# Kernel optimization log

Hardware: AMD Instinct MI355X
Metric: run time of the kernel (lower is better)

The kernel has to match this reference:

```python
import jax, jax.numpy as jnp
import numpy as np

T, B, E, H = 2048, 2, 1024, 16
HD = E // H
EPS = 1e-5


def setup_inputs() -> dict:
    key = jax.random.key(0)
    k1, k2, k3 = jax.random.split(key, 3)
    bound_in = float(np.sqrt(6.0 / (3 * E + E)))   # xavier_uniform for [3E,E]
    bound_out = float(np.sqrt(6.0 / (E + E)))      # xavier_uniform for [E,E]
    return {
        "query": jax.random.normal(k1, (T, B, E), dtype=jnp.float32),
        "gamma": jnp.ones((E,), dtype=jnp.float32),
        "beta": jnp.zeros((E,), dtype=jnp.float32),
        "in_proj_weight": jax.random.uniform(k2, (3 * E, E), jnp.float32, -bound_in, bound_in),
        "out_proj_weight": jax.random.uniform(k3, (E, E), jnp.float32, -bound_out, bound_out),
    }


def reference(query, gamma, beta, in_proj_weight, out_proj_weight):
    # LayerNorm over channel dim
    mean = jnp.mean(query, axis=-1, keepdims=True)
    var = jnp.mean(jnp.square(query - mean), axis=-1, keepdims=True)
    ln = (query - mean) * jax.lax.rsqrt(var + EPS) * gamma + beta  # [T,B,E]

    # Fused QKV projection (no bias): qkv = ln @ W^T, W: [3E, E]
    qkv = jnp.einsum("tbe,fe->tbf", ln, in_proj_weight)  # [T,B,3E]
    q, k, v = jnp.split(qkv, 3, axis=-1)
    q = q.reshape(T, B, H, HD) * (HD ** -0.5)
    k = k.reshape(T, B, H, HD)
    v = v.reshape(T, B, H, HD)

    # Attention: scores [B,H,T,T]
    scores = jnp.einsum("tbhd,sbhd->bhts", q, k)
    attn = jax.nn.softmax(scores, axis=-1)
    ctx = jnp.einsum("bhts,sbhd->tbhd", attn, v).reshape(T, B, E)

    # Output projection + residual add (dropout prob = 0)
    out = jnp.einsum("tbe,fe->tbf", ctx, out_proj_weight)
    return query + out
```

## Files before the change

### kernel.cpp

```cpp
#include <hip/hip_runtime.h>
#include <hip/hip_bf16.h>
#include <math.h>

#define T_DIM 2048
#define B_DIM 2
#define E_DIM 1024
#define H_DIM 16
#define HD_DIM 64
#define M_DIM (T_DIM * B_DIM)
#define BH_DIM (B_DIM * H_DIM)

using bf16x8 = __attribute__((ext_vector_type(8))) __bf16;
using u16x8  = __attribute__((ext_vector_type(8))) unsigned short;
using f32x4  = __attribute__((ext_vector_type(4))) float;

static __device__ __forceinline__ unsigned short f2bf(float f) {
  unsigned u = __builtin_bit_cast(unsigned, f);
  u += 0x7fff + ((u >> 16) & 1);
  return (unsigned short)(u >> 16);
}

__device__ __forceinline__ void gload_lds16(const void* g, void* l) {
  __builtin_amdgcn_global_load_lds(
      (const __attribute__((address_space(1))) unsigned int*)g,
      (__attribute__((address_space(3))) unsigned int*)l, 16, 0, 0);
}

__global__ __launch_bounds__(256) void prep_kernel(
    const float* __restrict__ q, const float* __restrict__ gamma,
    const float* __restrict__ beta, unsigned short* __restrict__ ln_out,
    const float* __restrict__ w1, unsigned short* __restrict__ o1, int n1,
    const float* __restrict__ w2, unsigned short* __restrict__ o2, int n2) {
  int blk = blockIdx.x;
  int tid = threadIdx.x;
  if (blk >= M_DIM) {
    int i = (blk - M_DIM) * 256 + tid;
    const float* in; unsigned short* out; int idx;
    if (i < n1) { in = w1; out = o1; idx = i; }
    else if (i < n1 + n2) { in = w2; out = o2; idx = i - n1; }
    else return;
    float4 v = ((const float4*)in)[idx];
    ushort4 o;
    o.x = f2bf(v.x); o.y = f2bf(v.y); o.z = f2bf(v.z); o.w = f2bf(v.w);
    ((ushort4*)out)[idx] = o;
    return;
  }
  int row = blk;
  const float4* qr = (const float4*)(q + (size_t)row * E_DIM);
  float4 x = qr[tid];
  float s  = x.x + x.y + x.z + x.w;
  float ss = x.x * x.x + x.y * x.y + x.z * x.z + x.w * x.w;
#pragma unroll
  for (int off = 32; off >= 1; off >>= 1) {
    s  += __shfl_xor(s, off, 64);
    ss += __shfl_xor(ss, off, 64);
  }
  __shared__ float red[8];
  int wid = tid >> 6, lane = tid & 63;
  if (lane == 0) { red[wid] = s; red[4 + wid] = ss; }
  __syncthreads();
  s  = red[0] + red[1] + red[2] + red[3];
  ss = red[4] + red[5] + red[6] + red[7];
  float mean = s * (1.0f / E_DIM);
  float var  = ss * (1.0f / E_DIM) - mean * mean;
  float rstd = rsqrtf(var + 1e-5f);
  float4 g4 = ((const float4*)gamma)[tid];
  float4 b4 = ((const float4*)beta)[tid];
  ushort4 o;
  o.x = f2bf((x.x - mean) * rstd * g4.x + b4.x);
  o.y = f2bf((x.y - mean) * rstd * g4.y + b4.y);
  o.z = f2bf((x.z - mean) * rstd * g4.z + b4.z);
  o.w = f2bf((x.w - mean) * rstd * g4.w + b4.w);
  ((ushort4*)(ln_out + (size_t)row * E_DIM))[tid] = o;
}

__global__ __launch_bounds__(512) void gemm0_kernel(
    const unsigned short* __restrict__ A, const unsigned short* __restrict__ Bw,
    unsigned short* __restrict__ out_qkv) {
  __shared__ alignas(16) unsigned short lds[65536];
  int tid = threadIdx.x;
  int wid = tid >> 6, lane = tid & 63;
  int wm = wid >> 2, wn = wid & 3;
  int g = lane >> 4, lr = lane & 15;
  int m0 = blockIdx.y * 256, n0 = blockIdx.x * 256;
  f32x4 acc[8][4] = {};
  bf16x8 bfr[4][2];

  int srl  = tid >> 3;
  int scol = ((tid & 7) ^ (srl & 7)) * 8;
  int koff0 = ((0 * 4 + g) ^ (lr & 7)) * 8;
  int koff1 = ((1 * 4 + g) ^ (lr & 7)) * 8;
  int bhalf = wn >> 1;
  int brow  = (wn & 1) * 64;

#define STAGE_HALF(PTR, GR0, KT, LBASE)                                        \
  do {                                                                         \
    gload_lds16((PTR) + (size_t)((GR0) + srl) * E_DIM + (size_t)(KT) * 64 + scol, \
                lds + (LBASE) + (size_t)tid * 8);                              \
    gload_lds16((PTR) + (size_t)((GR0) + 64 + srl) * E_DIM + (size_t)(KT) * 64 + scol, \
                lds + (LBASE) + 4096 + (size_t)tid * 8);                       \
  } while (0)

#define AOFF(D, MR, KK) (((D) * 2 + wm) * 8192 + ((MR) * 16 + lr) * 64 + ((KK) ? koff1 : koff0))
#define BOFF(D, NF, KK) (32768 + ((D) * 2 + bhalf) * 8192 + (brow + (NF) * 16 + lr) * 64 + ((KK) ? koff1 : koff0))

#define PHASE(Q, D, DOB, VW, ...)                                              \
  do {                                                                         \
    bf16x8 af[2][2];                                                           \
    _Pragma("unroll")                                                          \
    for (int mi = 0; mi < 2; ++mi) {                                           \
      af[mi][0] = *(const bf16x8*)(lds + AOFF(D, 2 * (Q) + mi, 0));            \
      af[mi][1] = *(const bf16x8*)(lds + AOFF(D, 2 * (Q) + mi, 1));            \
    }                                                                          \
    if (DOB) {                                                                 \
      _Pragma("unroll")                                                        \
      for (int nf = 0; nf < 4; ++nf) {                                         \
        bfr[nf][0] = *(const bf16x8*)(lds + BOFF(D, nf, 0));                   \
        bfr[nf][1] = *(const bf16x8*)(lds + BOFF(D, nf, 1));                   \
      }                                                                        \
    }                                                                          \
    __VA_ARGS__;                                                               \
    VW;                                                                        \
    __builtin_amdgcn_s_barrier();                                              \
    __builtin_amdgcn_sched_barrier(0);                                         \
    __builtin_amdgcn_s_setprio(1);                                             \
    _Pragma("unroll")                                                          \
    for (int mi = 0; mi < 2; ++mi)                                             \
      _Pragma("unroll")                                                        \
      for (int nf = 0; nf < 4; ++nf) {                                         \
        acc[2 * (Q) + mi][nf] = __builtin_amdgcn_mfma_f32_16x16x32_bf16(       \
            af[mi][0], bfr[nf][0], acc[2 * (Q) + mi][nf], 0, 0, 0);            \
        acc[2 * (Q) + mi][nf] = __builtin_amdgcn_mfma_f32_16x16x32_bf16(       \
            af[mi][1], bfr[nf][1], acc[2 * (Q) + mi][nf], 0, 0, 0);            \
      }                                                                        \
    __builtin_amdgcn_s_setprio(0);                                             \
    __builtin_amdgcn_s_barrier();                                              \
    __builtin_amdgcn_sched_barrier(0);                                         \
  } while (0)

#define VMC4 asm volatile("s_waitcnt vmcnt(4)" ::: "memory")
#define VMC0 asm volatile("s_waitcnt vmcnt(0)" ::: "memory")
#define NOWAIT ((void)0)

  STAGE_HALF(Bw, n0,       0, 32768);
  STAGE_HALF(Bw, n0 + 128, 0, 40960);
  STAGE_HALF(A,  m0,       0, 0);
  STAGE_HALF(A,  m0 + 128, 0, 8192);
  STAGE_HALF(Bw, n0,       1, 49152);
  STAGE_HALF(Bw, n0 + 128, 1, 57344);
  VMC0;
  __builtin_amdgcn_s_barrier();
  __builtin_amdgcn_sched_barrier(0);

  for (int i = 0; i < 7; ++i) {
    int k1 = 2 * i + 1, k2 = 2 * i + 2, k3 = 2 * i + 3;
    PHASE(0, 0, true,  NOWAIT, STAGE_HALF(A,  m0,       k1, 16384));
    PHASE(1, 0, false, NOWAIT, STAGE_HALF(A,  m0 + 128, k1, 24576));
    PHASE(2, 0, false, NOWAIT, STAGE_HALF(Bw, n0,       k2, 32768));
    PHASE(3, 0, false, VMC4,   STAGE_HALF(Bw, n0 + 128, k2, 40960));
    PHASE(0, 1, true,  NOWAIT, STAGE_HALF(A,  m0,       k2, 0));
    PHASE(1, 1, false, NOWAIT, STAGE_HALF(A,  m0 + 128, k2, 8192));
    PHASE(2, 1, false, NOWAIT, STAGE_HALF(Bw, n0,       k3, 49152));
    PHASE(3, 1, false, VMC4,   STAGE_HALF(Bw, n0 + 128, k3, 57344));
  }
  PHASE(0, 0, true,  NOWAIT, STAGE_HALF(A,  m0,       15, 16384));
  PHASE(1, 0, false, NOWAIT, STAGE_HALF(A,  m0 + 128, 15, 24576));
  PHASE(2, 0, false, NOWAIT, );
  PHASE(3, 0, false, VMC0,   );
  PHASE(0, 1, true,  NOWAIT, );
  PHASE(1, 1, false, NOWAIT, );
  PHASE(2, 1, false, NOWAIT, );
  PHASE(3, 1, false, NOWAIT, );
#undef PHASE
#undef STAGE_HALF
#undef AOFF
#undef BOFF
#undef VMC4
#undef VMC0
#undef NOWAIT

#pragma unroll
  for (int mr = 0; mr < 8; ++mr) {
#pragma unroll
    for (int nf = 0; nf < 4; ++nf) {
#pragma unroll
      for (int r = 0; r < 4; ++r) {
        int grow = m0 + wm * 128 + mr * 16 + g * 4 + r;
        int gcol = n0 + wn * 64 + nf * 16 + lr;
        int which = gcol >> 10, rem = gcol & 1023;
        int h = rem >> 6, d = rem & 63;
        int t = grow >> 1, b = grow & 1;
        out_qkv[(size_t)which * (BH_DIM * T_DIM * HD_DIM) +
                ((size_t)(b * H_DIM + h) * T_DIM + t) * HD_DIM + d] =
            f2bf(acc[mr][nf][r]);
      }
    }
  }
}

__global__ __launch_bounds__(256) void gemm1_kernel(
    const unsigned short* __restrict__ A, const unsigned short* __restrict__ Bw,
    const float* __restrict__ resid, float* __restrict__ out) {
  __shared__ alignas(16) unsigned short lA[3][128 * 32];
  __shared__ alignas(16) unsigned short lB[3][64 * 32];
  int tid = threadIdx.x;
  int wid = tid >> 6, lane = tid & 63;
  int g = lane >> 4, lr = lane & 15;
  int m0 = blockIdx.y * 128, n0 = blockIdx.x * 64;
  f32x4 acc[2][4] = {};

  int srcRow[2], srcCol[2];
#pragma unroll
  for (int c = 0; c < 2; ++c) {
    int n = c * 256 + tid;
    int laR = n >> 3, l = (n & 7) ^ (laR & 7);
    srcRow[c] = laR * 2 + (l >> 2);
    srcCol[c] = (l & 3) * 8;
  }
  int rs = (lr >> 1) & 7;
  int physc = ((((lr & 1) << 2) | g)) ^ rs;
  int fragA = (wid * 16 + (lr >> 1)) * 64 + physc * 8;
  int fragB = ((lr >> 1)) * 64 + physc * 8;

#define STAGE_G1(BUF, K0)                                                      \
  do {                                                                         \
    _Pragma("unroll")                                                          \
    for (int c = 0; c < 2; ++c)                                                \
      gload_lds16(A + (size_t)(m0 + srcRow[c]) * E_DIM + (K0) + srcCol[c],     \
                  lA[BUF] + (size_t)(c * 256 + wid * 64) * 8);                 \
    gload_lds16(Bw + (size_t)(n0 + srcRow[0]) * E_DIM + (K0) + srcCol[0],      \
                lB[BUF] + (size_t)(wid * 64) * 8);                             \
  } while (0)

#define PROCG1(BUF, NBUF, KK, LAST)                                            \
  do {                                                                         \
    if (!(LAST)) {                                                             \
      STAGE_G1(NBUF, ((KK) + 1) * 32);                                         \
      asm volatile("s_waitcnt vmcnt(3)" ::: "memory");                         \
    } else {                                                                   \
      asm volatile("s_waitcnt vmcnt(0)" ::: "memory");                         \
    }                                                                          \
    __builtin_amdgcn_s_barrier();                                              \
    __builtin_amdgcn_sched_barrier(0);                                         \
    bf16x8 af[2], bfr[4];                                                      \
    _Pragma("unroll")                                                          \
    for (int r = 0; r < 2; ++r)                                                \
      af[r] = *(const bf16x8*)(lA[BUF] + fragA + r * 512);                     \
    _Pragma("unroll")                                                          \
    for (int r = 0; r < 4; ++r)                                                \
      bfr[r] = *(const bf16x8*)(lB[BUF] + fragB + r * 512);                    \
    __builtin_amdgcn_s_setprio(1);                                             \
    _Pragma("unroll")                                                          \
    for (int mr = 0; mr < 2; ++mr)                                             \
      _Pragma("unroll")                                                        \
      for (int nr = 0; nr < 4; ++nr)                                           \
        acc[mr][nr] = __builtin_amdgcn_mfma_f32_16x16x32_bf16(                 \
            af[mr], bfr[nr], acc[mr][nr], 0, 0, 0);                            \
    __builtin_amdgcn_s_setprio(0);                                             \
  } while (0)

  STAGE_G1(0, 0);
  for (int kk = 0; kk < 30; kk += 3) {
    PROCG1(0, 1, kk + 0, false);
    PROCG1(1, 2, kk + 1, false);
    PROCG1(2, 0, kk + 2, false);
  }
  PROCG1(0, 1, 30, false);
  PROCG1(1, 2, 31, true);
#undef PROCG1
#undef STAGE_G1

#pragma unroll
  for (int mr = 0; mr < 2; ++mr) {
#pragma unroll
    for (int nr = 0; nr < 4; ++nr) {
#pragma unroll
      for (int r = 0; r < 4; ++r) {
        int grow = m0 + wid * 32 + mr * 16 + g * 4 + r;
        int gcol = n0 + nr * 16 + lr;
        size_t idx = (size_t)grow * E_DIM + gcol;
        out[idx] = resid[idx] + acc[mr][nr][r];
      }
    }
  }
}

__global__ __launch_bounds__(256) void transpose_v_kernel(
    const unsigned short* __restrict__ vb, unsigned short* __restrict__ vt) {
  __shared__ alignas(16) unsigned short tl[64 * 72];
  int tid = threadIdx.x;
  int bh = blockIdx.y, t0 = blockIdx.x * 64;
  const unsigned short* src = vb + ((size_t)bh * T_DIM + t0) * HD_DIM;
#pragma unroll
  for (int e = 0; e < 2; ++e) {
    int i8 = e * 256 + tid;
    int r = i8 >> 3;
    int c = (i8 & 7) * 8;
    int hsh = (r ^ (r >> 3)) & 7;
    bf16x8 v = *(const bf16x8*)(src + (size_t)r * HD_DIM + c);
    *(bf16x8*)(tl + r * 72 + (c ^ (hsh << 3))) = v;
  }
  __syncthreads();
  unsigned short* dst = vt + (size_t)bh * HD_DIM * T_DIM + t0;
#pragma unroll
  for (int e = 0; e < 2; ++e) {
    int i8 = e * 256 + tid;
    int d = i8 >> 3;
    int tc = (i8 & 7) * 8;
    u16x8 o;
#pragma unroll
    for (int j = 0; j < 8; ++j) {
      int p = tc + j;
      int ks = p >> 5, gg = (p >> 3) & 3, jl = p & 7;
      int r = (ks * 2 + (jl >> 2)) * 16 + gg * 4 + (jl & 3);
      int hsh = (r ^ (r >> 3)) & 7;
      o[j] = tl[r * 72 + (d ^ (hsh << 3))];
    }
    *(u16x8*)(dst + (size_t)d * T_DIM + tc) = o;
  }
}

__global__ __launch_bounds__(256) void attn_kernel(
    const unsigned short* __restrict__ qb, const unsigned short* __restrict__ kb,
    const unsigned short* __restrict__ vt, unsigned short* __restrict__ ctx) {
  __shared__ alignas(16) unsigned short lK[4][64 * 64];
  __shared__ alignas(16) unsigned short lV[4][64 * 64];
  int tid = threadIdx.x;
  int wid = tid >> 6, lane = tid & 63;
  int g = lane >> 4, lr = lane & 15;
  int f = blockIdx.x;
  int xcd = f & 7, rest = f >> 3;
  int bh = xcd + 8 * (rest & 3);
  int qt = rest >> 2;
  int b = bh >> 4, h = bh & 15;
  const size_t koff = (size_t)bh * T_DIM * HD_DIM;
  const size_t voff = (size_t)bh * HD_DIM * T_DIM;

  int srow = tid >> 3;
  int gch  = (tid & 7) ^ (srow & 7);
  const unsigned short* ks0 = kb + koff + (size_t)srow * HD_DIM + gch * 8;
  const unsigned short* vs0 = vt + voff + (size_t)srow * T_DIM + gch * 8;

#define STAGE_TILE(buf, T)                                                     \
  do {                                                                         \
    size_t kofs = (size_t)(T) * 64 * HD_DIM;                                   \
    size_t vofs = (size_t)(T) * 64;                                            \
    gload_lds16(ks0 + kofs,                 lK[buf] + wid * 512);              \
    gload_lds16(ks0 + kofs + 32 * HD_DIM,   lK[buf] + 2048 + wid * 512);       \
    gload_lds16(vs0 + vofs,                 lV[buf] + wid * 512);              \
    gload_lds16(vs0 + vofs + (size_t)32 * T_DIM, lV[buf] + 2048 + wid * 512);  \
  } while (0)

  bf16x8 qf[2][2];
  {
    const float QS = 0.125f * 1.44269504f;
#pragma unroll
    for (int qa = 0; qa < 2; ++qa) {
      int qrow = qt * 128 + wid * 32 + qa * 16 + lr;
#pragma unroll
      for (int ks = 0; ks < 2; ++ks) {
        bf16x8 raw = *(const bf16x8*)(qb + koff + (size_t)qrow * HD_DIM + ks * 32 + g * 8);
#pragma unroll
        for (int j = 0; j < 8; ++j) qf[qa][ks][j] = (__bf16)((float)raw[j] * QS);
      }
    }
  }

  bf16x8 onesf;
#pragma unroll
  for (int j = 0; j < 8; ++j) onesf[j] = (__bf16)1.0f;

  f32x4 accO[2][4] = {};
  f32x4 accS[2] = {};

#define COMPUTE_TILE(B)                                                        \
  do {                                                                         \
    const unsigned short* Kc = lK[B];                                          \
    const unsigned short* Vc = lV[B];                                          \
    f32x4 s4[2][4];                                                            \
    __builtin_amdgcn_s_setprio(1);                                             \
    _Pragma("unroll")                                                          \
    for (int cf = 0; cf < 4; ++cf) {                                           \
      int row = cf * 16 + lr;                                                  \
      int sw = (row & 7) << 3;                                                 \
      bf16x8 k0 = *(const bf16x8*)(Kc + row * 64 + ((g * 8) ^ sw));            \
      bf16x8 k1 = *(const bf16x8*)(Kc + row * 64 + ((32 + g * 8) ^ sw));       \
      _Pragma("unroll")                                                        \
      for (int qa = 0; qa < 2; ++qa) {                                         \
        f32x4 s = {-8.0f, -8.0f, -8.0f, -8.0f};                                \
        s = __builtin_amdgcn_mfma_f32_16x16x32_bf16(k0, qf[qa][0], s, 0, 0, 0);\
        s = __builtin_amdgcn_mfma_f32_16x16x32_bf16(k1, qf[qa][1], s, 0, 0, 0);\
        s4[qa][cf] = s;                                                        \
      }                                                                        \
    }                                                                          \
    __builtin_amdgcn_s_setprio(0);                                             \
    bf16x8 pf[2][2];                                                           \
    _Pragma("unroll")                                                          \
    for (int qa = 0; qa < 2; ++qa)                                             \
      _Pragma("unroll")                                                        \
      for (int j = 0; j < 8; ++j) {                                            \
        pf[qa][0][j] = (__bf16)__builtin_amdgcn_exp2f(s4[qa][(j >> 2)][j & 3]);\
        pf[qa][1][j] = (__bf16)__builtin_amdgcn_exp2f(s4[qa][2 + (j >> 2)][j & 3]);\
      }                                                                        \
    __builtin_amdgcn_s_setprio(1);                                             \
    _Pragma("unroll")                                                          \
    for (int ks = 0; ks < 2; ++ks) {                                           \
      _Pragma("unroll")                                                        \
      for (int qa = 0; qa < 2; ++qa)                                           \
        accS[qa] = __builtin_amdgcn_mfma_f32_16x16x32_bf16(onesf, pf[qa][ks], accS[qa], 0, 0, 0); \
      _Pragma("unroll")                                                        \
      for (int df = 0; df < 4; ++df) {                                         \
        int row = df * 16 + lr;                                                \
        int sw = (row & 7) << 3;                                               \
        bf16x8 vf = *(const bf16x8*)(Vc + row * 64 + ((ks * 32 + g * 8) ^ sw));\
        _Pragma("unroll")                                                      \
        for (int qa = 0; qa < 2; ++qa)                                         \
          accO[qa][df] = __builtin_amdgcn_mfma_f32_16x16x32_bf16(vf, pf[qa][ks], accO[qa][df], 0, 0, 0); \
      }                                                                        \
    }                                                                          \
    __builtin_amdgcn_s_setprio(0);                                             \
  } while (0)

#define INTERVAL(BA, BB, SA, SB, TT, STG)                                      \
  do {                                                                         \
    asm volatile("s_waitcnt vmcnt(0)" ::: "memory");                           \
    __builtin_amdgcn_s_barrier();                                              \
    __builtin_amdgcn_sched_barrier(0);                                         \
    if (STG) {                                                                 \
      STAGE_TILE(SA, (TT) + 2);                                                \
      STAGE_TILE(SB, (TT) + 3);                                                \
    }                                                                          \
    COMPUTE_TILE(BA);                                                          \
    COMPUTE_TILE(BB);                                                          \
  } while (0)

  STAGE_TILE(0, 0);
  STAGE_TILE(1, 1);
  for (int tt = 0; tt < 28; tt += 4) {
    INTERVAL(0, 1, 2, 3, tt, true);
    INTERVAL(2, 3, 0, 1, tt + 2, true);
  }
  INTERVAL(0, 1, 2, 3, 28, true);
  INTERVAL(2, 3, 0, 1, 30, false);
#undef INTERVAL
#undef COMPUTE_TILE
#undef STAGE_TILE

  __syncthreads();
  unsigned short* sc = (unsigned short*)lK + wid * (32 * 72);
  float invl[2];
  invl[0] = 1.0f / accS[0][0];
  invl[1] = 1.0f / accS[1][0];
#pragma unroll
  for (int qa = 0; qa < 2; ++qa)
#pragma unroll
    for (int df = 0; df < 4; ++df)
#pragma unroll
      for (int r = 0; r < 4; ++r)
        sc[(qa * 16 + lr) * 72 + df * 16 + g * 4 + r] =
            f2bf(accO[qa][df][r] * invl[qa]);
  __syncthreads();
#pragma unroll
  for (int i = 0; i < 4; ++i) {
    int idx = i * 64 + lane;
    int row = idx >> 3, ch = idx & 7;
    u16x8 v8 = *(const u16x8*)(sc + row * 72 + ch * 8);
    int t = qt * 128 + wid * 32 + row;
    *(u16x8*)(&ctx[((size_t)t * B_DIM + b) * E_DIM + h * HD_DIM + ch * 8]) = v8;
  }
}

extern "C" void kernel_launch(void* const* d_in, const int* in_sizes, int n_in,
                              void* d_out, int out_size, void* d_ws, size_t ws_size,
                              hipStream_t stream) {
  const float* query = (const float*)d_in[0];
  const float* gamma = (const float*)d_in[1];
  const float* beta  = (const float*)d_in[2];
  const float* w_in  = (const float*)d_in[3];
  const float* w_out = (const float*)d_in[4];
  float* out = (float*)d_out;

  unsigned short* ws    = (unsigned short*)d_ws;
  unsigned short* ln    = ws;
  unsigned short* winb  = ln + (size_t)M_DIM * E_DIM;
  unsigned short* woutb = winb + (size_t)3 * E_DIM * E_DIM;
  unsigned short* qkv   = woutb + (size_t)E_DIM * E_DIM;

  unsigned short* qbuf = qkv;
  unsigned short* kbuf = qkv + (size_t)BH_DIM * T_DIM * HD_DIM;
  unsigned short* vbuf = kbuf + (size_t)BH_DIM * T_DIM * HD_DIM;
  unsigned short* vtb  = ln;
  unsigned short* ctx  = vbuf;

  prep_kernel<<<dim3(M_DIM + 4096), dim3(256), 0, stream>>>(
      query, gamma, beta, ln,
      w_in, winb, 3 * E_DIM * E_DIM / 4, w_out, woutb, E_DIM * E_DIM / 4);
  gemm0_kernel<<<dim3(3 * E_DIM / 256, M_DIM / 256), dim3(512), 0, stream>>>(
      ln, winb, qkv);
  transpose_v_kernel<<<dim3(T_DIM / 64, BH_DIM), dim3(256), 0, stream>>>(vbuf, vtb);
  attn_kernel<<<dim3(512), dim3(256), 0, stream>>>(qbuf, kbuf, vtb, ctx);
  gemm1_kernel<<<dim3(E_DIM / 64, M_DIM / 128), dim3(256), 0, stream>>>(
      ctx, woutb, query, out);
}
```

Measured before the change: 113.9 us.

## Switch attention MFMAs from 16x16x32 to 32x32x16 tiles

Reworks the attention inner loop to use 32x32x16 bf16 MFMA instructions instead of 16x16x32, so each wave computes its 32 query rows as single 32-wide tiles. The Q fragments, the K/V LDS read pattern, the exp/P fragment layout and the V-transpose permutation are all changed to match the 32x32 operand layout. The aim is fewer MFMA issues and fewer LDS fragment loads per tile, which improves operand reuse. In exchange it needs larger accumulator register arrays (f32x16), which may raise register pressure.

Measured after the change: 120.2 us. +5.5%, slower.

```diff
diff --git a/kernel.cpp b/kernel.cpp
--- a/kernel.cpp
+++ b/kernel.cpp
@@ -13,6 +13,7 @@
 using bf16x8 = __attribute__((ext_vector_type(8))) __bf16;
 using u16x8  = __attribute__((ext_vector_type(8))) unsigned short;
 using f32x4  = __attribute__((ext_vector_type(4))) float;
+using f32x16 = __attribute__((ext_vector_type(16))) float;
 
 static __device__ __forceinline__ unsigned short f2bf(float f) {
   unsigned u = __builtin_bit_cast(unsigned, f);
@@ -311,8 +312,7 @@
 #pragma unroll
     for (int j = 0; j < 8; ++j) {
       int p = tc + j;
-      int ks = p >> 5, gg = (p >> 3) & 3, jl = p & 7;
-      int r = (ks * 2 + (jl >> 2)) * 16 + gg * 4 + (jl & 3);
+      int r = (p & 51) | ((p & 4) << 1) | ((p & 8) >> 1);
       int hsh = (r ^ (r >> 3)) & 7;
       o[j] = tl[r * 72 + (d ^ (hsh << 3))];
     }
@@ -327,7 +327,7 @@
   __shared__ alignas(16) unsigned short lV[4][64 * 64];
   int tid = threadIdx.x;
   int wid = tid >> 6, lane = tid & 63;
-  int g = lane >> 4, lr = lane & 15;
+  int l31 = lane & 31, hi = lane >> 5;
   int f = blockIdx.x;
   int xcd = f & 7, rest = f >> 3;
   int bh = xcd + 8 * (rest & 3);
@@ -351,18 +351,15 @@
     gload_lds16(vs0 + vofs + (size_t)32 * T_DIM, lV[buf] + 2048 + wid * 512);  \
   } while (0)
 
-  bf16x8 qf[2][2];
+  bf16x8 qf[4];
   {
     const float QS = 0.125f * 1.44269504f;
-#pragma unroll
-    for (int qa = 0; qa < 2; ++qa) {
-      int qrow = qt * 128 + wid * 32 + qa * 16 + lr;
-#pragma unroll
-      for (int ks = 0; ks < 2; ++ks) {
-        bf16x8 raw = *(const bf16x8*)(qb + koff + (size_t)qrow * HD_DIM + ks * 32 + g * 8);
-#pragma unroll
-        for (int j = 0; j < 8; ++j) qf[qa][ks][j] = (__bf16)((float)raw[j] * QS);
-      }
+    int qrow = qt * 128 + wid * 32 + l31;
+#pragma unroll
+    for (int c = 0; c < 4; ++c) {
+      bf16x8 raw = *(const bf16x8*)(qb + koff + (size_t)qrow * HD_DIM + c * 16 + hi * 8);
+#pragma unroll
+      for (int j = 0; j < 8; ++j) qf[c][j] = (__bf16)((float)raw[j] * QS);
     }
   }
 
@@ -370,52 +367,47 @@
 #pragma unroll
   for (int j = 0; j < 8; ++j) onesf[j] = (__bf16)1.0f;
 
-  f32x4 accO[2][4] = {};
-  f32x4 accS[2] = {};
+  f32x16 accO[2] = {};
+  f32x16 accS = {};
 
 #define COMPUTE_TILE(B)                                                        \
   do {                                                                         \
     const unsigned short* Kc = lK[B];                                          \
     const unsigned short* Vc = lV[B];                                          \
-    f32x4 s4[2][4];                                                            \
+    f32x16 s32[2];                                                             \
     __builtin_amdgcn_s_setprio(1);                                             \
     _Pragma("unroll")                                                          \
-    for (int cf = 0; cf < 4; ++cf) {                                           \
-      int row = cf * 16 + lr;                                                  \
-      int sw = (row & 7) << 3;                                                 \
-      bf16x8 k0 = *(const bf16x8*)(Kc + row * 64 + ((g * 8) ^ sw));            \
-      bf16x8 k1 = *(const bf16x8*)(Kc + row * 64 + ((32 + g * 8) ^ sw));       \
-      _Pragma("unroll")                                                        \
-      for (int qa = 0; qa < 2; ++qa) {                                         \
-        f32x4 s = {-8.0f, -8.0f, -8.0f, -8.0f};                                \
-        s = __builtin_amdgcn_mfma_f32_16x16x32_bf16(k0, qf[qa][0], s, 0, 0, 0);\
-        s = __builtin_amdgcn_mfma_f32_16x16x32_bf16(k1, qf[qa][1], s, 0, 0, 0);\
-        s4[qa][cf] = s;                                                        \
+    for (int kt2 = 0; kt2 < 2; ++kt2) {                                        \
+      int row = kt2 * 32 + l31;                                                \
+      int sw = row & 7;                                                        \
+      f32x16 s = {-8.0f, -8.0f, -8.0f, -8.0f, -8.0f, -8.0f, -8.0f, -8.0f,      \
+                  -8.0f, -8.0f, -8.0f, -8.0f, -8.0f, -8.0f, -8.0f, -8.0f};     \
+      _Pragma("unroll")                                                        \
+      for (int c = 0; c < 4; ++c) {                                            \
+        bf16x8 ka = *(const bf16x8*)(Kc + row * 64 + ((c * 2 + hi) ^ sw) * 8); \
+        s = __builtin_amdgcn_mfma_f32_32x32x16_bf16(ka, qf[c], s, 0, 0, 0);    \
       }                                                                        \
+      s32[kt2] = s;                                                            \
     }                                                                          \
     __builtin_amdgcn_s_setprio(0);                                             \
-    bf16x8 pf[2][2];                                                           \
-    _Pragma("unroll")                                                          \
-    for (int qa = 0; qa < 2; ++qa)                                             \
-      _Pragma("unroll")                                                        \
-      for (int j = 0; j < 8; ++j) {                                            \
-        pf[qa][0][j] = (__bf16)__builtin_amdgcn_exp2f(s4[qa][(j >> 2)][j & 3]);\
-        pf[qa][1][j] = (__bf16)__builtin_amdgcn_exp2f(s4[qa][2 + (j >> 2)][j & 3]);\
-      }                                                                        \
+    bf16x8 pf[4];                                                              \
+    _Pragma("unroll")                                                          \
+    for (int sl = 0; sl < 4; ++sl)                                             \
+      _Pragma("unroll")                                                        \
+      for (int j = 0; j < 8; ++j)                                              \
+        pf[sl][j] = (__bf16)__builtin_amdgcn_exp2f(s32[sl >> 1][8 * (sl & 1) + j]); \
     __builtin_amdgcn_s_setprio(1);                                             \
     _Pragma("unroll")                                                          \
-    for (int ks = 0; ks < 2; ++ks) {                                           \
-      _Pragma("unroll")                                                        \
-      for (int qa = 0; qa < 2; ++qa)                                           \
-        accS[qa] = __builtin_amdgcn_mfma_f32_16x16x32_bf16(onesf, pf[qa][ks], accS[qa], 0, 0, 0); \
-      _Pragma("unroll")                                                        \
-      for (int df = 0; df < 4; ++df) {                                         \
-        int row = df * 16 + lr;                                                \
-        int sw = (row & 7) << 3;                                               \
-        bf16x8 vf = *(const bf16x8*)(Vc + row * 64 + ((ks * 32 + g * 8) ^ sw));\
-        _Pragma("unroll")                                                      \
-        for (int qa = 0; qa < 2; ++qa)                                         \
-          accO[qa][df] = __builtin_amdgcn_mfma_f32_16x16x32_bf16(vf, pf[qa][ks], accO[qa][df], 0, 0, 0); \
+    for (int sl = 0; sl < 4; ++sl)                                             \
+      accS = __builtin_amdgcn_mfma_f32_32x32x16_bf16(onesf, pf[sl], accS, 0, 0, 0); \
+    _Pragma("unroll")                                                          \
+    for (int dt = 0; dt < 2; ++dt) {                                           \
+      int row = dt * 32 + l31;                                                 \
+      int sw = row & 7;                                                        \
+      _Pragma("unroll")                                                        \
+      for (int sl = 0; sl < 4; ++sl) {                                         \
+        bf16x8 va = *(const bf16x8*)(Vc + row * 64 + ((sl * 2 + hi) ^ sw) * 8);\
+        accO[dt] = __builtin_amdgcn_mfma_f32_32x32x16_bf16(va, pf[sl], accO[dt], 0, 0, 0); \
       }                                                                        \
     }                                                                          \
     __builtin_amdgcn_s_setprio(0);                                             \
@@ -448,17 +440,14 @@
 
   __syncthreads();
   unsigned short* sc = (unsigned short*)lK + wid * (32 * 72);
-  float invl[2];
-  invl[0] = 1.0f / accS[0][0];
-  invl[1] = 1.0f / accS[1][0];
-#pragma unroll
-  for (int qa = 0; qa < 2; ++qa)
-#pragma unroll
-    for (int df = 0; df < 4; ++df)
-#pragma unroll
-      for (int r = 0; r < 4; ++r)
-        sc[(qa * 16 + lr) * 72 + df * 16 + g * 4 + r] =
-            f2bf(accO[qa][df][r] * invl[qa]);
+  float invl = 1.0f / accS[0];
+#pragma unroll
+  for (int dt = 0; dt < 2; ++dt)
+#pragma unroll
+    for (int reg = 0; reg < 16; ++reg) {
+      int d = dt * 32 + (reg & 3) + 8 * (reg >> 2) + 4 * hi;
+      sc[l31 * 72 + d] = f2bf(accO[dt][reg] * invl);
+    }
   __syncthreads();
 #pragma unroll
   for (int i = 0; i < 4; ++i) {
```
